# Performance work log

Measured on AMD Instinct MI355X. Metric: run time of the kernel, lower is better.

The kernel has to match this reference:

```python
import jax, jax.numpy as jnp
import numpy as np

SEQ, B, IN, H, OUT, L = 256, 64, 512, 1024, 256, 2
DT = 0.05

def setup_inputs() -> dict:
    key = jax.random.key(0)
    ks = jax.random.split(key, 10)
    s = lambda fan_in: 1.0 / np.sqrt(fan_in)
    return {
        "x":    jax.random.normal(ks[0], (SEQ, B, IN), dtype=jnp.float32),
        "W_in": jax.random.uniform(ks[1], (H, IN), jnp.float32, -s(IN), s(IN)),
        "b_in": jax.random.uniform(ks[2], (H,), jnp.float32, -s(IN), s(IN)),
        "W_c":  jax.random.uniform(ks[3], (H, 2 * H), jnp.float32, -s(2 * H), s(2 * H)),
        "b_c":  jax.random.uniform(ks[4], (H,), jnp.float32, -s(2 * H), s(2 * H)),
        "taus": jnp.ones((L,), jnp.float32),
        "W_o1": jax.random.uniform(ks[5], (H // 2, H), jnp.float32, -s(H), s(H)),
        "b_o1": jax.random.uniform(ks[6], (H // 2,), jnp.float32, -s(H), s(H)),
        "W_o2": jax.random.uniform(ks[7], (OUT, H // 2), jnp.float32, -s(H // 2), s(H // 2)),
        "b_o2": jax.random.uniform(ks[8], (OUT,), jnp.float32, -s(H // 2), s(H // 2)),
    }

def reference(x, W_in, b_in, W_c, b_c, taus, W_o1, b_o1, W_o2, b_o2):
    # input projection for all timesteps at once: [S,B,IN] -> [S,B,H]
    xp = jnp.einsum('sbi,hi->sbh', x, W_in) + b_in
    num_layers = taus.shape[0]
    batch = x.shape[1]
    hidden0 = jnp.zeros((num_layers, batch, W_in.shape[0]), dtype=x.dtype)

    def step(hidden, xt):
        inp = xt  # [B,H]
        new_hidden = []
        for layer in range(num_layers):
            h = hidden[layer]
            # original code calls cell(input_t.detach(), h): stop gradient on input path
            comb = jnp.concatenate([jax.lax.stop_gradient(inp), h], axis=-1)  # [B,2H]
            dhdt = jnp.tanh(comb @ W_c.T + b_c)
            h_next = h + (DT / (taus[layer] + 0.001)) * dhdt
            new_hidden.append(h_next)
            inp = h_next
        hidden = jnp.stack(new_hidden)  # [L,B,H]
        out = jax.nn.relu(hidden[-1] @ W_o1.T + b_o1) @ W_o2.T + b_o2  # [B,OUT]
        return hidden, out

    hidden_final, outputs = jax.lax.scan(step, hidden0, xp)
    return outputs, hidden_final
```

## Files before the change

### kernel.cpp

```cpp
#include <hip/hip_runtime.h>
#include <hip/hip_bf16.h>
#include <stdint.h>

typedef unsigned short ushort_t;
typedef unsigned long long ull_t;
using bf16x8 = __attribute__((ext_vector_type(8))) short;
using f32x4  = __attribute__((ext_vector_type(4))) float;

#define SEQ    256
#define BATCH  64
#define INDIM  512
#define HDIM   1024
#define OUTDIM 256
#define MTOT   (SEQ*BATCH)
#define BH     (BATCH*HDIM)

__device__ __forceinline__ ushort_t f2bf(float f) {
  uint32_t u = __builtin_bit_cast(uint32_t, f);
  u += 0x7fffu + ((u >> 16) & 1u);
  return (ushort_t)(u >> 16);
}
__device__ __forceinline__ float bf2f(ushort_t b) {
  uint32_t u = ((uint32_t)b) << 16;
  return __builtin_bit_cast(float, u);
}
__device__ __forceinline__ f32x4 mfma16(bf16x8 a, bf16x8 b, f32x4 c) {
  return __builtin_amdgcn_mfma_f32_16x16x32_bf16(a, b, c, 0, 0, 0);
}
__device__ __forceinline__ void gload16(const void* g, void* l) {
  __builtin_amdgcn_global_load_lds(
      (const __attribute__((address_space(1))) unsigned int*)g,
      (__attribute__((address_space(3))) unsigned int*)l, 16, 0, 0);
}
__device__ __forceinline__ float tanhfast(float z) {
  float e = __expf(2.0f * z);
  return 1.0f - 2.0f / (e + 1.0f);
}
__device__ __forceinline__ ull_t pack4bf(const float* v) {
  ull_t p = 0;
#pragma unroll
  for (int j = 0; j < 4; ++j) p |= (ull_t)f2bf(v[j]) << (16 * j);
  return p;
}
__device__ __forceinline__ int load_sc0_int(const int* p) {
  int v;
  asm volatile("global_load_dword %0, %1, off sc0\n\ts_waitcnt vmcnt(0)"
               : "=&v"(v) : "v"(p) : "memory");
  return v;
}

__global__ void k_convert(const float* __restrict__ src, ushort_t* __restrict__ dst, int n) {
  int i = blockIdx.x * blockDim.x + threadIdx.x;
  if (i < n) dst[i] = f2bf(src[i]);
}
__global__ void k_split(const float* __restrict__ src, ushort_t* __restrict__ hi,
                        ushort_t* __restrict__ lo, int n) {
  int i = blockIdx.x * blockDim.x + threadIdx.x;
  if (i < n) {
    float v = src[i];
    ushort_t h = f2bf(v);
    hi[i] = h;
    lo[i] = f2bf(v - bf2f(h));
  }
}
__global__ void k_split_wc(const float* __restrict__ Wc,
                           ushort_t* __restrict__ WiH, ushort_t* __restrict__ WiL,
                           ushort_t* __restrict__ WhH, ushort_t* __restrict__ WhL) {
  int i = blockIdx.x * blockDim.x + threadIdx.x;
  if (i < HDIM * HDIM) {
    int row = i >> 10, k = i & 1023;
    float vi = Wc[(size_t)row * (2 * HDIM) + k];
    float vh = Wc[(size_t)row * (2 * HDIM) + HDIM + k];
    ushort_t ih = f2bf(vi);
    WiH[i] = ih; WiL[i] = f2bf(vi - bf2f(ih));
    ushort_t hh = f2bf(vh);
    WhH[i] = hh; WhL[i] = f2bf(vh - bf2f(hh));
  }
}

template<int SPLITB, int RELU, int OUTBF>
__global__ __launch_bounds__(256) void gemm_nt(
    const ushort_t* __restrict__ A, const ushort_t* __restrict__ Bhi,
    const ushort_t* __restrict__ Blo, const float* __restrict__ bias,
    float* __restrict__ Cf, ushort_t* __restrict__ Cb,
    int M, int N, int K)
{
  __shared__ ushort_t As[128 * 32];
  __shared__ ushort_t Bh[128 * 32];
  __shared__ ushort_t Bl[128 * 32];
  const int tid = threadIdx.x;
  const int w = tid >> 6, l = tid & 63;
  const int m0 = blockIdx.x * 128, n0 = blockIdx.y * 128;
  const int wr = w >> 1, wc = w & 1;
  const int lr = l & 15, lk = l >> 4;

  f32x4 acc[4][4] = {};
  const int nK = K >> 5;
  const size_t rowB = (size_t)K * 2;

  for (int kk = 0; kk < nK; ++kk) {
    const size_t kbyte = (size_t)kk * 64;
#pragma unroll
    for (int j = 0; j < 2; ++j) {
      int c = (w * 2 + j) * 64 + l;
      int row = c >> 2;
      int kb = (c & 3) * 16;
      gload16((const char*)A + (size_t)(m0 + row) * rowB + kbyte + kb,
              (char*)As + (w * 2 + j) * 1024);
      gload16((const char*)Bhi + (size_t)(n0 + row) * rowB + kbyte + kb,
              (char*)Bh + (w * 2 + j) * 1024);
      if (SPLITB)
        gload16((const char*)Blo + (size_t)(n0 + row) * rowB + kbyte + kb,
                (char*)Bl + (w * 2 + j) * 1024);
    }
    __syncthreads();
    bf16x8 af[4], bhf[4], blf[4];
#pragma unroll
    for (int i = 0; i < 4; ++i) {
      af[i]  = *(const bf16x8*)&As[(wr * 64 + i * 16 + lr) * 32 + lk * 8];
      bhf[i] = *(const bf16x8*)&Bh[(wc * 64 + i * 16 + lr) * 32 + lk * 8];
      if (SPLITB)
        blf[i] = *(const bf16x8*)&Bl[(wc * 64 + i * 16 + lr) * 32 + lk * 8];
    }
#pragma unroll
    for (int i = 0; i < 4; ++i)
#pragma unroll
      for (int j2 = 0; j2 < 4; ++j2) {
        acc[i][j2] = mfma16(af[i], bhf[j2], acc[i][j2]);
        if (SPLITB) acc[i][j2] = mfma16(af[i], blf[j2], acc[i][j2]);
      }
    __syncthreads();
  }
#pragma unroll
  for (int j2 = 0; j2 < 4; ++j2) {
    int n = n0 + wc * 64 + j2 * 16 + lr;
    float bv = bias ? bias[n] : 0.0f;
#pragma unroll
    for (int i = 0; i < 4; ++i) {
#pragma unroll
      for (int r = 0; r < 4; ++r) {
        int m = m0 + wr * 64 + i * 16 + lk * 4 + r;
        float v = acc[i][j2][r] + bv;
        if (RELU) v = fmaxf(v, 0.0f);
        if (OUTBF) Cb[(size_t)m * N + n] = f2bf(v);
        else       Cf[(size_t)m * N + n] = v;
      }
    }
  }
}

__global__ __attribute__((amdgpu_waves_per_eu(2, 2))) __launch_bounds__(512)
void scan_kernel(
    const float* __restrict__ P0,
    const ushort_t* __restrict__ WiH, const ushort_t* __restrict__ WiL,
    const ushort_t* __restrict__ WhH, const ushort_t* __restrict__ WhL,
    const float* __restrict__ b_c, const float* __restrict__ taus,
    ushort_t* __restrict__ h0buf,
    ushort_t* __restrict__ H1buf,
    float* __restrict__ outHidden, int* __restrict__ sync)
{
  __shared__ float red[2][2][8][64][11];
  __shared__ int meta[2];

  const int tid = threadIdx.x;
  const int w = tid >> 6, l = tid & 63;
  const int lr = l & 15, lk = l >> 4;

  int* cnt        = sync;
  int* flags_l2   = sync + 64;
  int* flags_mall = sync + 192;

  if (tid == 0) {
    int xcd;
    asm volatile("s_getreg_b32 %0, hwreg(HW_REG_XCC_ID)" : "=s"(xcd));
    int slot = 999;
    if (xcd < 4)
      slot = __hip_atomic_fetch_add(&cnt[xcd], 1, __ATOMIC_RELAXED,
                                    __HIP_MEMORY_SCOPE_AGENT);
    meta[0] = (xcd < 4) ? xcd : -1;
    meta[1] = slot;
  }
  __syncthreads();
  const int g = meta[0];
  const int c = meta[1];
  if (g < 0 || c >= 32) return;

  const int rowg = g * 16, colg = c * 32;
  const int kb = w * 128;

  bf16x8 whh[2][4], whl[2][4], wih[2][4], wil[2][4];
#pragma unroll
  for (int ct = 0; ct < 2; ++ct)
#pragma unroll
    for (int kk = 0; kk < 4; ++kk) {
      size_t off = (size_t)(colg + ct * 16 + lr) * HDIM + kb + kk * 32 + lk * 8;
      whh[ct][kk] = *(const bf16x8*)&WhH[off];
      whl[ct][kk] = *(const bf16x8*)&WhL[off];
      wih[ct][kk] = *(const bf16x8*)&WiH[off];
      wil[ct][kk] = *(const bf16x8*)&WiL[off];
    }

  const int R = l >> 2, jc = (l & 3) * 4;
  const int lo_base = 16 * (l >> 4);
  const int ro = (l >> 2) & 3;
  float hm0[4] = {0, 0, 0, 0}, hm1[4] = {0, 0, 0, 0};
  float bc4[4] = {0, 0, 0, 0};
  float a0c = 0.f, a1c = 0.f;
  float4 p0v = make_float4(0.f, 0.f, 0.f, 0.f);
  if (w < 2) {
#pragma unroll
    for (int j = 0; j < 4; ++j) bc4[j] = b_c[colg + w * 16 + jc + j];
    a0c = 0.05f / (taus[0] + 0.001f);
    a1c = 0.05f / (taus[1] + 0.001f);
    p0v = *(const float4*)&P0[((size_t)0 * BATCH + rowg + R) * HDIM + colg + w * 16 + jc];
  }

  for (int i = 0; i <= SEQ; ++i) {
    bf16x8 f[4], hh[4];
    f32x4 aA[2] = {}, aI[2] = {}, aH[2] = {};

    if (i >= 1) {
      const ushort_t* h0r = h0buf + (size_t)(i - 1) * BH;
#pragma unroll
      for (int kk = 0; kk < 4; ++kk)
        f[kk] = *(const bf16x8*)&h0r[(size_t)(rowg + lr) * HDIM + kb + kk * 32 + lk * 8];
      if (i >= 2) {
        const ushort_t* h1r = H1buf + (size_t)(i - 2) * BH;
#pragma unroll
        for (int kk = 0; kk < 4; ++kk)
          hh[kk] = *(const bf16x8*)&h1r[(size_t)(rowg + lr) * HDIM + kb + kk * 32 + lk * 8];
      }
#pragma unroll
      for (int kk = 0; kk < 4; ++kk)
#pragma unroll
        for (int ct = 0; ct < 2; ++ct) {
          aA[ct] = mfma16(f[kk], whh[ct][kk], aA[ct]);
          aA[ct] = mfma16(f[kk], whl[ct][kk], aA[ct]);
          aI[ct] = mfma16(f[kk], wih[ct][kk], aI[ct]);
          aI[ct] = mfma16(f[kk], wil[ct][kk], aI[ct]);
        }
      if (i >= 2) {
#pragma unroll
        for (int kk = 0; kk < 4; ++kk)
#pragma unroll
          for (int ct = 0; ct < 2; ++ct) {
            aH[ct] = mfma16(hh[kk], whh[ct][kk], aH[ct]);
            aH[ct] = mfma16(hh[kk], whl[ct][kk], aH[ct]);
          }
      }
    }
#pragma unroll
    for (int ct = 0; ct < 2; ++ct)
#pragma unroll
      for (int r = 0; r < 4; ++r) {
        red[0][ct][w][l][r] = aA[ct][r];
        red[1][ct][w][l][r] = aI[ct][r] + aH[ct][r];
      }
    __syncthreads();

    if (w < 2) {
      float sA[4], sB[4];
#pragma unroll
      for (int j = 0; j < 4; ++j) {
        const int src = jc + j + lo_base;
        float s0 = 0.f, s1 = 0.f;
#pragma unroll
        for (int q = 0; q < 8; ++q) {
          s0 += red[0][w][q][src][ro];
          s1 += red[1][w][q][src][ro];
        }
        sA[j] = s0; sB[j] = s1;
      }
      if (i < SEQ) {
        float p4[4] = {p0v.x, p0v.y, p0v.z, p0v.w};
#pragma unroll
        for (int j = 0; j < 4; ++j) hm0[j] += a0c * tanhfast(p4[j] + sA[j]);
        *(ull_t*)&h0buf[(size_t)i * BH + (size_t)(rowg + R) * HDIM +
                        colg + w * 16 + jc] = pack4bf(hm0);
      }
      if (i >= 1) {
#pragma unroll
        for (int j = 0; j < 4; ++j) hm1[j] += a1c * tanhfast(sB[j] + bc4[j]);
        *(ull_t*)&H1buf[(size_t)(i - 1) * BH + (size_t)(rowg + R) * HDIM +
                        colg + w * 16 + jc] = pack4bf(hm1);
      }
      asm volatile("s_waitcnt vmcnt(0)" ::: "memory");
    }
    __syncthreads();

    if (i < SEQ) {
      if (tid == 0) {
        *(volatile int*)&flags_l2[g * 32 + c] = i + 1;
        asm volatile("" ::: "memory");
        __hip_atomic_store(&flags_mall[g * 32 + c], i + 1, __ATOMIC_RELAXED,
                           __HIP_MEMORY_SCOPE_AGENT);
      }
      if (w < 2 && i + 1 < SEQ)
        p0v = *(const float4*)&P0[((size_t)(i + 1) * BATCH + rowg + R) * HDIM +
                                  colg + w * 16 + jc];
      if (w == 2) {
        const int target = i + 1;
        const int* fl2 = &flags_l2[g * 32 + (l & 31)];
        int* fml = &flags_mall[g * 32 + (l & 31)];
        for (int r = 0;; ++r) {
          int v = ((r & 3) == 3)
            ? __hip_atomic_load(fml, __ATOMIC_RELAXED, __HIP_MEMORY_SCOPE_AGENT)
            : load_sc0_int(fl2);
          if (__all(v >= target)) break;
        }
      }
      __syncthreads();
    }
  }

  if (w < 2) {
    float4 o0 = make_float4(hm0[0], hm0[1], hm0[2], hm0[3]);
    float4 o1 = make_float4(hm1[0], hm1[1], hm1[2], hm1[3]);
    *(float4*)&outHidden[(size_t)(rowg + R) * HDIM + colg + w * 16 + jc] = o0;
    *(float4*)&outHidden[(size_t)BH + (size_t)(rowg + R) * HDIM + colg + w * 16 + jc] = o1;
  }
}

extern "C" void kernel_launch(void* const* d_in, const int* in_sizes, int n_in,
                              void* d_out, int out_size, void* d_ws, size_t ws_size,
                              hipStream_t stream) {
  const float* x    = (const float*)d_in[0];
  const float* W_in = (const float*)d_in[1];
  const float* b_in = (const float*)d_in[2];
  const float* W_c  = (const float*)d_in[3];
  const float* b_c  = (const float*)d_in[4];
  const float* taus = (const float*)d_in[5];
  const float* W_o1 = (const float*)d_in[6];
  const float* b_o1 = (const float*)d_in[7];
  const float* W_o2 = (const float*)d_in[8];
  const float* b_o2 = (const float*)d_in[9];
  float* out = (float*)d_out;

  char* ws = (char*)d_ws;
  size_t off = 0;
  auto alloc = [&](size_t bytes) -> char* {
    char* p = ws + off;
    off += (bytes + 255) & ~(size_t)255;
    return p;
  };
  ushort_t* x_bf  = (ushort_t*)alloc((size_t)MTOT * INDIM * 2);
  ushort_t* xp_b  = (ushort_t*)alloc((size_t)MTOT * HDIM * 2);
  float*    P0    = (float*)   alloc((size_t)MTOT * HDIM * 4);
  ushort_t* H1buf = (ushort_t*)alloc((size_t)MTOT * HDIM * 2);
  ushort_t* h0buf = (ushort_t*)alloc((size_t)SEQ * BH * 2);
  ushort_t* O1    = (ushort_t*)alloc((size_t)MTOT * (HDIM/2) * 2);
  ushort_t* WiH   = (ushort_t*)alloc((size_t)HDIM * HDIM * 2);
  ushort_t* WiL   = (ushort_t*)alloc((size_t)HDIM * HDIM * 2);
  ushort_t* WhH   = (ushort_t*)alloc((size_t)HDIM * HDIM * 2);
  ushort_t* WhL   = (ushort_t*)alloc((size_t)HDIM * HDIM * 2);
  ushort_t* WinH  = (ushort_t*)alloc((size_t)HDIM * INDIM * 2);
  ushort_t* WinL  = (ushort_t*)alloc((size_t)HDIM * INDIM * 2);
  ushort_t* Wo1b  = (ushort_t*)alloc((size_t)(HDIM/2) * HDIM * 2);
  ushort_t* Wo2b  = (ushort_t*)alloc((size_t)OUTDIM * (HDIM/2) * 2);
  int*      sync  = (int*)     alloc(4096);
  if (off > ws_size) return;

  hipMemsetAsync(sync, 0, 4096, stream);

  k_convert<<<(MTOT * INDIM + 255) / 256, 256, 0, stream>>>(x, x_bf, MTOT * INDIM);
  k_split<<<(HDIM * INDIM + 255) / 256, 256, 0, stream>>>(W_in, WinH, WinL, HDIM * INDIM);
  k_split_wc<<<(HDIM * HDIM + 255) / 256, 256, 0, stream>>>(W_c, WiH, WiL, WhH, WhL);
  k_convert<<<((HDIM/2) * HDIM + 255) / 256, 256, 0, stream>>>(W_o1, Wo1b, (HDIM/2) * HDIM);
  k_convert<<<(OUTDIM * (HDIM/2) + 255) / 256, 256, 0, stream>>>(W_o2, Wo2b, OUTDIM * (HDIM/2));

  gemm_nt<1, 0, 1><<<dim3(MTOT / 128, HDIM / 128), 256, 0, stream>>>(
      x_bf, WinH, WinL, b_in, nullptr, xp_b, MTOT, HDIM, INDIM);
  gemm_nt<1, 0, 0><<<dim3(MTOT / 128, HDIM / 128), 256, 0, stream>>>(
      xp_b, WiH, WiL, b_c, P0, nullptr, MTOT, HDIM, HDIM);

  scan_kernel<<<512, 512, 0, stream>>>(P0, WiH, WiL, WhH, WhL, b_c, taus,
                                       h0buf, H1buf,
                                       out + (size_t)SEQ * BATCH * OUTDIM, sync);

  gemm_nt<0, 1, 1><<<dim3(MTOT / 128, (HDIM/2) / 128), 256, 0, stream>>>(
      H1buf, Wo1b, nullptr, b_o1, nullptr, O1, MTOT, HDIM / 2, HDIM);
  gemm_nt<0, 0, 0><<<dim3(MTOT / 128, OUTDIM / 128), 256, 0, stream>>>(
      O1, Wo2b, nullptr, b_o2, out, nullptr, MTOT, OUTDIM, HDIM / 2);
}
```

Measured before the change: 1.331 ms.

## Split scan K-reduction across 16 waves and spread epilogue over four waves

The persistent scan kernel grows from 512 to 1024 threads per block. Each wave now covers a 64-wide K slice instead of 128, so the serial MFMA chain and the register-resident weight footprint per wave are halved. The cross-wave reduction buffer is relaid out for vectorized f32x4 writes and reads. The two-layer epilogue moves from two waves to four, one layer per wave pair, so the tanh and store work per step runs in parallel. In exchange, the per-step reduction sums 16 partials instead of 8, the launch_bounds change may alter register allocation, and stores now go out as scalar bf16 rather than packed 64-bit writes.

```diff
diff --git a/kernel.cpp b/kernel.cpp
--- a/kernel.cpp
+++ b/kernel.cpp
@@ -35,12 +35,6 @@
 __device__ __forceinline__ float tanhfast(float z) {
   float e = __expf(2.0f * z);
   return 1.0f - 2.0f / (e + 1.0f);
-}
-__device__ __forceinline__ ull_t pack4bf(const float* v) {
-  ull_t p = 0;
-#pragma unroll
-  for (int j = 0; j < 4; ++j) p |= (ull_t)f2bf(v[j]) << (16 * j);
-  return p;
 }
 __device__ __forceinline__ int load_sc0_int(const int* p) {
   int v;
@@ -149,8 +143,7 @@
   }
 }
 
-__global__ __attribute__((amdgpu_waves_per_eu(2, 2))) __launch_bounds__(512)
-void scan_kernel(
+__global__ __launch_bounds__(1024, 4) void scan_kernel(
     const float* __restrict__ P0,
     const ushort_t* __restrict__ WiH, const ushort_t* __restrict__ WiL,
     const ushort_t* __restrict__ WhH, const ushort_t* __restrict__ WhL,
@@ -159,7 +152,7 @@
     ushort_t* __restrict__ H1buf,
     float* __restrict__ outHidden, int* __restrict__ sync)
 {
-  __shared__ float red[2][2][8][64][11];
+  __shared__ float red[4 * 16 * 320];
   __shared__ int meta[2];
 
   const int tid = threadIdx.x;
@@ -186,13 +179,13 @@
   if (g < 0 || c >= 32) return;
 
   const int rowg = g * 16, colg = c * 32;
-  const int kb = w * 128;
-
-  bf16x8 whh[2][4], whl[2][4], wih[2][4], wil[2][4];
+  const int kb = w * 64;
+
+  bf16x8 whh[2][2], whl[2][2], wih[2][2], wil[2][2];
 #pragma unroll
   for (int ct = 0; ct < 2; ++ct)
 #pragma unroll
-    for (int kk = 0; kk < 4; ++kk) {
+    for (int kk = 0; kk < 2; ++kk) {
       size_t off = (size_t)(colg + ct * 16 + lr) * HDIM + kb + kk * 32 + lk * 8;
       whh[ct][kk] = *(const bf16x8*)&WhH[off];
       whl[ct][kk] = *(const bf16x8*)&WhL[off];
@@ -200,89 +193,93 @@
       wil[ct][kk] = *(const bf16x8*)&WiL[off];
     }
 
-  const int R = l >> 2, jc = (l & 3) * 4;
-  const int lo_base = 16 * (l >> 4);
-  const int ro = (l >> 2) & 3;
-  float hm0[4] = {0, 0, 0, 0}, hm1[4] = {0, 0, 0, 0};
-  float bc4[4] = {0, 0, 0, 0};
-  float a0c = 0.f, a1c = 0.f;
-  float4 p0v = make_float4(0.f, 0.f, 0.f, 0.f);
-  if (w < 2) {
-#pragma unroll
-    for (int j = 0; j < 4; ++j) bc4[j] = b_c[colg + w * 16 + jc + j];
-    a0c = 0.05f / (taus[0] + 0.001f);
-    a1c = 0.05f / (taus[1] + 0.001f);
-    p0v = *(const float4*)&P0[((size_t)0 * BATCH + rowg + R) * HDIM + colg + w * 16 + jc];
+  const int ep = (w < 4);
+  const int ph = w >> 1, ect = w & 1;
+  const int ec = lr, R0 = lk * 4;
+  float hm[4] = {0, 0, 0, 0};
+  float bcn = 0.f, alpha = 0.f;
+  float p0r[4] = {0, 0, 0, 0};
+  if (ep) {
+    alpha = 0.05f / (taus[ph] + 0.001f);
+    bcn = b_c[colg + ect * 16 + ec];
+    if (ph == 0) {
+#pragma unroll
+      for (int j = 0; j < 4; ++j)
+        p0r[j] = P0[((size_t)0 * BATCH + rowg + R0 + j) * HDIM + colg + ect * 16 + ec];
+    }
   }
 
   for (int i = 0; i <= SEQ; ++i) {
-    bf16x8 f[4], hh[4];
+#pragma unroll
+    for (int ct = 0; ct < 2; ++ct)
+#pragma unroll
+      for (int kk = 0; kk < 2; ++kk)
+        asm volatile("" : "+v"(whh[ct][kk]), "+v"(whl[ct][kk]),
+                          "+v"(wih[ct][kk]), "+v"(wil[ct][kk]));
+
+    bf16x8 f0 = {}, f1 = {}, g0 = {}, g1 = {};
     f32x4 aA[2] = {}, aI[2] = {}, aH[2] = {};
-
     if (i >= 1) {
       const ushort_t* h0r = h0buf + (size_t)(i - 1) * BH;
-#pragma unroll
-      for (int kk = 0; kk < 4; ++kk)
-        f[kk] = *(const bf16x8*)&h0r[(size_t)(rowg + lr) * HDIM + kb + kk * 32 + lk * 8];
+      f0 = *(const bf16x8*)&h0r[(size_t)(rowg + lr) * HDIM + kb + lk * 8];
+      f1 = *(const bf16x8*)&h0r[(size_t)(rowg + lr) * HDIM + kb + 32 + lk * 8];
       if (i >= 2) {
         const ushort_t* h1r = H1buf + (size_t)(i - 2) * BH;
-#pragma unroll
-        for (int kk = 0; kk < 4; ++kk)
-          hh[kk] = *(const bf16x8*)&h1r[(size_t)(rowg + lr) * HDIM + kb + kk * 32 + lk * 8];
-      }
-#pragma unroll
-      for (int kk = 0; kk < 4; ++kk)
+        g0 = *(const bf16x8*)&h1r[(size_t)(rowg + lr) * HDIM + kb + lk * 8];
+        g1 = *(const bf16x8*)&h1r[(size_t)(rowg + lr) * HDIM + kb + 32 + lk * 8];
+      }
+#pragma unroll
+      for (int ct = 0; ct < 2; ++ct) {
+        aA[ct] = mfma16(f0, whh[ct][0], aA[ct]);
+        aA[ct] = mfma16(f0, whl[ct][0], aA[ct]);
+        aA[ct] = mfma16(f1, whh[ct][1], aA[ct]);
+        aA[ct] = mfma16(f1, whl[ct][1], aA[ct]);
+        aI[ct] = mfma16(f0, wih[ct][0], aI[ct]);
+        aI[ct] = mfma16(f0, wil[ct][0], aI[ct]);
+        aI[ct] = mfma16(f1, wih[ct][1], aI[ct]);
+        aI[ct] = mfma16(f1, wil[ct][1], aI[ct]);
+      }
+      if (i >= 2) {
 #pragma unroll
         for (int ct = 0; ct < 2; ++ct) {
-          aA[ct] = mfma16(f[kk], whh[ct][kk], aA[ct]);
-          aA[ct] = mfma16(f[kk], whl[ct][kk], aA[ct]);
-          aI[ct] = mfma16(f[kk], wih[ct][kk], aI[ct]);
-          aI[ct] = mfma16(f[kk], wil[ct][kk], aI[ct]);
+          aH[ct] = mfma16(g0, whh[ct][0], aH[ct]);
+          aH[ct] = mfma16(g0, whl[ct][0], aH[ct]);
+          aH[ct] = mfma16(g1, whh[ct][1], aH[ct]);
+          aH[ct] = mfma16(g1, whl[ct][1], aH[ct]);
         }
-      if (i >= 2) {
-#pragma unroll
-        for (int kk = 0; kk < 4; ++kk)
-#pragma unroll
-          for (int ct = 0; ct < 2; ++ct) {
-            aH[ct] = mfma16(hh[kk], whh[ct][kk], aH[ct]);
-            aH[ct] = mfma16(hh[kk], whl[ct][kk], aH[ct]);
-          }
-      }
-    }
-#pragma unroll
-    for (int ct = 0; ct < 2; ++ct)
-#pragma unroll
-      for (int r = 0; r < 4; ++r) {
-        red[0][ct][w][l][r] = aA[ct][r];
-        red[1][ct][w][l][r] = aI[ct][r] + aH[ct][r];
-      }
+      }
+    }
+    const int wbase = lr * 20 + lk * 4;
+#pragma unroll
+    for (int ct = 0; ct < 2; ++ct) {
+      *(f32x4*)&red[((0 + ct) * 16 + w) * 320 + wbase] = aA[ct];
+      f32x4 pb = aI[ct] + aH[ct];
+      *(f32x4*)&red[((2 + ct) * 16 + w) * 320 + wbase] = pb;
+    }
     __syncthreads();
 
-    if (w < 2) {
-      float sA[4], sB[4];
-#pragma unroll
-      for (int j = 0; j < 4; ++j) {
-        const int src = jc + j + lo_base;
-        float s0 = 0.f, s1 = 0.f;
-#pragma unroll
-        for (int q = 0; q < 8; ++q) {
-          s0 += red[0][w][q][src][ro];
-          s1 += red[1][w][q][src][ro];
+    if (ep && ((ph == 0 && i < SEQ) || (ph == 1 && i >= 1))) {
+      f32x4 s = {};
+      const float* rb = &red[(w * 16) * 320 + ec * 20 + R0];
+#pragma unroll
+      for (int q = 0; q < 16; ++q)
+        s += *(const f32x4*)&rb[q * 320];
+      if (ph == 0) {
+        ushort_t* dst = &h0buf[(size_t)i * BH + (size_t)(rowg + R0) * HDIM +
+                               colg + ect * 16 + ec];
+#pragma unroll
+        for (int j = 0; j < 4; ++j) {
+          hm[j] += alpha * tanhfast(p0r[j] + s[j]);
+          dst[(size_t)j * HDIM] = f2bf(hm[j]);
         }
-        sA[j] = s0; sB[j] = s1;
-      }
-      if (i < SEQ) {
-        float p4[4] = {p0v.x, p0v.y, p0v.z, p0v.w};
-#pragma unroll
-        for (int j = 0; j < 4; ++j) hm0[j] += a0c * tanhfast(p4[j] + sA[j]);
-        *(ull_t*)&h0buf[(size_t)i * BH + (size_t)(rowg + R) * HDIM +
-                        colg + w * 16 + jc] = pack4bf(hm0);
-      }
-      if (i >= 1) {
-#pragma unroll
-        for (int j = 0; j < 4; ++j) hm1[j] += a1c * tanhfast(sB[j] + bc4[j]);
-        *(ull_t*)&H1buf[(size_t)(i - 1) * BH + (size_t)(rowg + R) * HDIM +
-                        colg + w * 16 + jc] = pack4bf(hm1);
+      } else {
+        ushort_t* dst = &H1buf[(size_t)(i - 1) * BH + (size_t)(rowg + R0) * HDIM +
+                               colg + ect * 16 + ec];
+#pragma unroll
+        for (int j = 0; j < 4; ++j) {
+          hm[j] += alpha * tanhfast(s[j] + bcn);
+          dst[(size_t)j * HDIM] = f2bf(hm[j]);
+        }
       }
       asm volatile("s_waitcnt vmcnt(0)" ::: "memory");
     }
@@ -295,10 +292,13 @@
         __hip_atomic_store(&flags_mall[g * 32 + c], i + 1, __ATOMIC_RELAXED,
                            __HIP_MEMORY_SCOPE_AGENT);
       }
-      if (w < 2 && i + 1 < SEQ)
-        p0v = *(const float4*)&P0[((size_t)(i + 1) * BATCH + rowg + R) * HDIM +
-                                  colg + w * 16 + jc];
-      if (w == 2) {
+      if (ep && ph == 0 && i + 1 < SEQ) {
+#pragma unroll
+        for (int j = 0; j < 4; ++j)
+          p0r[j] = P0[((size_t)(i + 1) * BATCH + rowg + R0 + j) * HDIM +
+                      colg + ect * 16 + ec];
+      }
+      if (w == 4) {
         const int target = i + 1;
         const int* fl2 = &flags_l2[g * 32 + (l & 31)];
         int* fml = &flags_mall[g * 32 + (l & 31)];
@@ -313,11 +313,11 @@
     }
   }
 
-  if (w < 2) {
-    float4 o0 = make_float4(hm0[0], hm0[1], hm0[2], hm0[3]);
-    float4 o1 = make_float4(hm1[0], hm1[1], hm1[2], hm1[3]);
-    *(float4*)&outHidden[(size_t)(rowg + R) * HDIM + colg + w * 16 + jc] = o0;
-    *(float4*)&outHidden[(size_t)BH + (size_t)(rowg + R) * HDIM + colg + w * 16 + jc] = o1;
+  if (ep) {
+    float* dst = &outHidden[(size_t)ph * BH + (size_t)(rowg + R0) * HDIM +
+                            colg + ect * 16 + ec];
+#pragma unroll
+    for (int j = 0; j < 4; ++j) dst[(size_t)j * HDIM] = hm[j];
   }
 }
 
@@ -373,9 +373,9 @@
   gemm_nt<1, 0, 0><<<dim3(MTOT / 128, HDIM / 128), 256, 0, stream>>>(
       xp_b, WiH, WiL, b_c, P0, nullptr, MTOT, HDIM, HDIM);
 
-  scan_kernel<<<512, 512, 0, stream>>>(P0, WiH, WiL, WhH, WhL, b_c, taus,
-                                       h0buf, H1buf,
-                                       out + (size_t)SEQ * BATCH * OUTDIM, sync);
+  scan_kernel<<<512, 1024, 0, stream>>>(P0, WiH, WiL, WhH, WhL, b_c, taus,
+                                        h0buf, H1buf,
+                                        out + (size_t)SEQ * BATCH * OUTDIM, sync);
 
   gemm_nt<0, 1, 1><<<dim3(MTOT / 128, (HDIM/2) / 128), 256, 0, stream>>>(
       H1buf, Wo1b, nullptr, b_o1, nullptr, O1, MTOT, HDIM / 2, HDIM);
```

New measurement: 1.226 ms (median of 2 runs). 1.09x faster.
